# Kernel tuning notes

Measured on AMD Instinct MI355X. Metric: run time of the kernel, lower is better.

Reference implementation:

```python
import jax, jax.numpy as jnp
import numpy as np


def setup_inputs() -> dict:
    key = jax.random.key(0)
    k1, k2 = jax.random.split(key)
    x = jax.random.normal(k1, (32, 512, 512, 1), dtype=jnp.float32)
    se = jnp.ones((3, 3), dtype=jnp.float32)
    rank = jax.random.normal(k2, (9,), dtype=jnp.float32)
    return {"x": x, "se": se, "rank": rank}


def _extract_patches_3x3_same(x):
    # x: [B, H, W, 1] -> [B, H, W, 9], zero-padded SAME, row-major window order
    B, H, W, C = x.shape
    xp = jnp.pad(x, ((0, 0), (1, 1), (1, 1), (0, 0)))
    shifts = [xp[:, dy:dy + H, dx:dx + W, 0] for dy in range(3) for dx in range(3)]
    return jnp.stack(shifts, axis=-1)  # [B, H, W, 9]


def reference(x, se, rank):
    # Faithful to Morph2D.call: patches * se, sort ascending over the 9-window,
    # softmax(rank)-weighted sum -> soft rank-order filter.
    patches = _extract_patches_3x3_same(x)              # [B,H,W,9]
    weighted = patches * se.reshape(9)                  # elementwise by SE
    sorted_p = jnp.sort(weighted, axis=-1)              # ascending over window
    w = jax.nn.softmax(rank)                            # [9]
    out = jnp.sum(sorted_p * w, axis=-1)                # [B,H,W]
    return out.reshape(x.shape)                         # [B,H,W,1]
```

## Files before the change

### kernel.cpp

```cpp
#include <hip/hip_runtime.h>


#define HH 512
#define WW 512

#define RFL(x) __int_as_float(__builtin_amdgcn_readfirstlane(__float_as_int(x)))
#define MIN3(a,b,c) fminf(fminf(a,b),c)
#define MAX3(a,b,c) fmaxf(fmaxf(a,b),c)
#define MED3(a,b,c) __builtin_amdgcn_fmed3f(a,b,c)
#define TSORT(a,b,c) { float t0_=MIN3(a,b,c), t1_=MED3(a,b,c), t2_=MAX3(a,b,c); a=t0_; b=t1_; c=t2_; }

__global__ __launch_bounds__(256) void morph2d_kernel(
    const float* __restrict__ x, const float* __restrict__ se9,
    const float* __restrict__ rank, float* __restrict__ out)
{
    int nper = gridDim.x >> 3;
    int lb   = (blockIdx.x & 7) * nper + (blockIdx.x >> 3);
    int g    = lb * 256 + threadIdx.x;

    int gx = g & 127;
    int rg = (g >> 7) & 127;
    int b  = g >> 14;
    int x4 = gx << 2;
    int y0 = rg << 2;
    int lane = threadIdx.x & 63;

    const float* img = x + (size_t)b * (HH * WW);

    int   rowoff[6];
    float mm[6];
    #pragma unroll
    for (int r = 0; r < 6; ++r) {
        int ry = y0 - 1 + r;
        rowoff[r] = min(max(ry, 0), HH - 1) * WW;
        mm[r]     = (ry >= 0 && ry < HH) ? 1.f : 0.f;
    }

    float4 c[6];
    #pragma unroll
    for (int r = 0; r < 6; ++r)
        c[r] = *(const float4*)(img + rowoff[r] + x4);

    bool eL = (lane == 0)  && (x4 > 0);
    bool eR = (lane == 63) && (x4 + 4 < WW);
    float eg[6] = {0.f, 0.f, 0.f, 0.f, 0.f, 0.f};
    if (eL || eR) {
        int eoff = eL ? (x4 - 1) : (x4 + 4);
        #pragma unroll
        for (int r = 0; r < 6; ++r)
            eg[r] = img[rowoff[r] + eoff];
    }

    float w0,w1,w2,w3,w4,w5,w6,w7,w8;
    float s0,s1,s2,s3,s4,s5,s6,s7,s8;
    {
        float e[9]; float s = 0.f;
        #pragma unroll
        for (int i = 0; i < 9; ++i) { e[i] = __expf(rank[i]); s += e[i]; }
        float inv = 1.0f / s;
        w0=RFL(e[0]*inv); w1=RFL(e[1]*inv); w2=RFL(e[2]*inv);
        w3=RFL(e[3]*inv); w4=RFL(e[4]*inv); w5=RFL(e[5]*inv);
        w6=RFL(e[6]*inv); w7=RFL(e[7]*inv); w8=RFL(e[8]*inv);
        s0=RFL(se9[0]); s1=RFL(se9[1]); s2=RFL(se9[2]); s3=RFL(se9[3]);
        s4=RFL(se9[4]); s5=RFL(se9[5]); s6=RFL(se9[6]); s7=RFL(se9[7]); s8=RFL(se9[8]);
    }

    float R[6][6];
    #pragma unroll
    for (int r = 0; r < 6; ++r) {
        float lw = __shfl_up(c[r].w, 1);
        float rx = __shfl_down(c[r].x, 1);
        float lf = (lane == 0)  ? eg[r] : lw;
        float rt = (lane == 63) ? eg[r] : rx;
        float m  = mm[r];
        R[r][0] = lf * m;     R[r][1] = c[r].x * m; R[r][2] = c[r].y * m;
        R[r][3] = c[r].z * m; R[r][4] = c[r].w * m; R[r][5] = rt * m;
    }

    #pragma unroll
    for (int r = 0; r < 4; ++r) {
        float res[4];
        #pragma unroll
        for (int j = 0; j < 4; ++j) {
            float v0 = R[r  ][j]*s0, v1 = R[r  ][j+1]*s1, v2 = R[r  ][j+2]*s2;
            float v3 = R[r+1][j]*s3, v4 = R[r+1][j+1]*s4, v5 = R[r+1][j+2]*s5;
            float v6 = R[r+2][j]*s6, v7 = R[r+2][j+1]*s7, v8 = R[r+2][j+2]*s8;

            TSORT(v0, v1, v2)
            TSORT(v3, v4, v5)
            TSORT(v6, v7, v8)
            TSORT(v0, v3, v6)
            TSORT(v1, v4, v7)
            TSORT(v2, v5, v8)
            float r1 = fminf(v1, v3), p = fmaxf(v1, v3);
            float r7 = fmaxf(v5, v7), q = fminf(v5, v7);
            TSORT(v2, v4, v6)
            float r2 = fminf(p, v2), r3 = fmaxf(p, v2);
            float r5 = fminf(q, v6), r6 = fmaxf(q, v6);

            float acc = v0 * w0;
            acc = fmaf(r1, w1, acc);
            acc = fmaf(r2, w2, acc);
            acc = fmaf(r3, w3, acc);
            acc = fmaf(v4, w4, acc);
            acc = fmaf(r5, w5, acc);
            acc = fmaf(r6, w6, acc);
            acc = fmaf(r7, w7, acc);
            acc = fmaf(v8, w8, acc);
            res[j] = acc;
        }
        float4 o = { res[0], res[1], res[2], res[3] };
        *(float4*)(out + (((size_t)b * HH + (y0 + r)) * WW + x4)) = o;
    }
}

extern "C" void kernel_launch(void* const* d_in, const int* in_sizes, int n_in,
                              void* d_out, int out_size, void* d_ws, size_t ws_size,
                              hipStream_t stream) {
    const float* x    = (const float*)d_in[0];
    const float* se   = (const float*)d_in[1];
    const float* rank = (const float*)d_in[2];
    float* out = (float*)d_out;

    const int total_threads = 32 * (HH / 4) * (WW / 4);
    morph2d_kernel<<<total_threads / 256, 256, 0, stream>>>(x, se, rank, out);
}
```

Baseline: 90.17 us.

## Add uniform-SE fast path sharing column sorts across adjacent outputs

Adds a branch, taken when all nine structuring-element values are equal and positive, that pulls the scale out of the sort and folds it into the softmax weights. In that branch each column of three is sorted once and the result is shared by the overlapping windows, so each output pixel needs only the row sorts and the final merge. The per-row multiply by a validity mask is replaced by zeroing the top or bottom halo row only at the image edges. The general path is kept for non-uniform SE values, at the cost of more code size and a few uniform comparisons per thread.

```diff
diff --git a/kernel.cpp b/kernel.cpp
--- a/kernel.cpp
+++ b/kernel.cpp
@@ -27,13 +27,11 @@
 
     const float* img = x + (size_t)b * (HH * WW);
 
-    int   rowoff[6];
-    float mm[6];
+    int rowoff[6];
     #pragma unroll
     for (int r = 0; r < 6; ++r) {
         int ry = y0 - 1 + r;
         rowoff[r] = min(max(ry, 0), HH - 1) * WW;
-        mm[r]     = (ry >= 0 && ry < HH) ? 1.f : 0.f;
     }
 
     float4 c[6];
@@ -72,45 +70,102 @@
         float rx = __shfl_down(c[r].x, 1);
         float lf = (lane == 0)  ? eg[r] : lw;
         float rt = (lane == 63) ? eg[r] : rx;
-        float m  = mm[r];
-        R[r][0] = lf * m;     R[r][1] = c[r].x * m; R[r][2] = c[r].y * m;
-        R[r][3] = c[r].z * m; R[r][4] = c[r].w * m; R[r][5] = rt * m;
+        R[r][0] = lf;     R[r][1] = c[r].x; R[r][2] = c[r].y;
+        R[r][3] = c[r].z; R[r][4] = c[r].w; R[r][5] = rt;
     }
 
-    #pragma unroll
-    for (int r = 0; r < 4; ++r) {
-        float res[4];
+    if (y0 == 0) {
         #pragma unroll
-        for (int j = 0; j < 4; ++j) {
-            float v0 = R[r  ][j]*s0, v1 = R[r  ][j+1]*s1, v2 = R[r  ][j+2]*s2;
-            float v3 = R[r+1][j]*s3, v4 = R[r+1][j+1]*s4, v5 = R[r+1][j+2]*s5;
-            float v6 = R[r+2][j]*s6, v7 = R[r+2][j+1]*s7, v8 = R[r+2][j+2]*s8;
+        for (int cc = 0; cc < 6; ++cc) R[0][cc] = 0.f;
+    }
+    if (y0 == HH - 4) {
+        #pragma unroll
+        for (int cc = 0; cc < 6; ++cc) R[5][cc] = 0.f;
+    }
 
-            TSORT(v0, v1, v2)
-            TSORT(v3, v4, v5)
-            TSORT(v6, v7, v8)
-            TSORT(v0, v3, v6)
-            TSORT(v1, v4, v7)
-            TSORT(v2, v5, v8)
-            float r1 = fminf(v1, v3), p = fmaxf(v1, v3);
-            float r7 = fmaxf(v5, v7), q = fminf(v5, v7);
-            TSORT(v2, v4, v6)
-            float r2 = fminf(p, v2), r3 = fmaxf(p, v2);
-            float r5 = fminf(q, v6), r6 = fmaxf(q, v6);
+    bool uni = (s0==s1) && (s1==s2) && (s2==s3) && (s3==s4) &&
+               (s4==s5) && (s5==s6) && (s6==s7) && (s7==s8) && (s0 > 0.f);
 
-            float acc = v0 * w0;
-            acc = fmaf(r1, w1, acc);
-            acc = fmaf(r2, w2, acc);
-            acc = fmaf(r3, w3, acc);
-            acc = fmaf(v4, w4, acc);
-            acc = fmaf(r5, w5, acc);
-            acc = fmaf(r6, w6, acc);
-            acc = fmaf(r7, w7, acc);
-            acc = fmaf(v8, w8, acc);
-            res[j] = acc;
+    if (uni) {
+        float W0=RFL(w0*s0), W1=RFL(w1*s0), W2=RFL(w2*s0);
+        float W3=RFL(w3*s0), W4=RFL(w4*s0), W5=RFL(w5*s0);
+        float W6=RFL(w6*s0), W7=RFL(w7*s0), W8=RFL(w8*s0);
+
+        #pragma unroll
+        for (int r = 0; r < 4; ++r) {
+            float cs0[6], cs1[6], cs2[6];
+            #pragma unroll
+            for (int cc = 0; cc < 6; ++cc) {
+                float u0 = R[r][cc], u1 = R[r+1][cc], u2 = R[r+2][cc];
+                TSORT(u0, u1, u2)
+                cs0[cc] = u0; cs1[cc] = u1; cs2[cc] = u2;
+            }
+            float res[4];
+            #pragma unroll
+            for (int j = 0; j < 4; ++j) {
+                float v0 = cs0[j], v1 = cs0[j+1], v2 = cs0[j+2];
+                float v3 = cs1[j], v4 = cs1[j+1], v5 = cs1[j+2];
+                float v6 = cs2[j], v7 = cs2[j+1], v8 = cs2[j+2];
+
+                TSORT(v0, v1, v2)
+                TSORT(v3, v4, v5)
+                TSORT(v6, v7, v8)
+                float r1 = fminf(v1, v3), p = fmaxf(v1, v3);
+                float r7 = fmaxf(v5, v7), q = fminf(v5, v7);
+                TSORT(v2, v4, v6)
+                float r2 = fminf(p, v2), r3 = fmaxf(p, v2);
+                float r5 = fminf(q, v6), r6 = fmaxf(q, v6);
+
+                float acc = v0 * W0;
+                acc = fmaf(r1, W1, acc);
+                acc = fmaf(r2, W2, acc);
+                acc = fmaf(r3, W3, acc);
+                acc = fmaf(v4, W4, acc);
+                acc = fmaf(r5, W5, acc);
+                acc = fmaf(r6, W6, acc);
+                acc = fmaf(r7, W7, acc);
+                acc = fmaf(v8, W8, acc);
+                res[j] = acc;
+            }
+            float4 o = { res[0], res[1], res[2], res[3] };
+            *(float4*)(out + (((size_t)b * HH + (y0 + r)) * WW + x4)) = o;
         }
-        float4 o = { res[0], res[1], res[2], res[3] };
-        *(float4*)(out + (((size_t)b * HH + (y0 + r)) * WW + x4)) = o;
+    } else {
+        #pragma unroll
+        for (int r = 0; r < 4; ++r) {
+            float res[4];
+            #pragma unroll
+            for (int j = 0; j < 4; ++j) {
+                float v0 = R[r  ][j]*s0, v1 = R[r  ][j+1]*s1, v2 = R[r  ][j+2]*s2;
+                float v3 = R[r+1][j]*s3, v4 = R[r+1][j+1]*s4, v5 = R[r+1][j+2]*s5;
+                float v6 = R[r+2][j]*s6, v7 = R[r+2][j+1]*s7, v8 = R[r+2][j+2]*s8;
+
+                TSORT(v0, v1, v2)
+                TSORT(v3, v4, v5)
+                TSORT(v6, v7, v8)
+                TSORT(v0, v3, v6)
+                TSORT(v1, v4, v7)
+                TSORT(v2, v5, v8)
+                float r1 = fminf(v1, v3), p = fmaxf(v1, v3);
+                float r7 = fmaxf(v5, v7), q = fminf(v5, v7);
+                TSORT(v2, v4, v6)
+                float r2 = fminf(p, v2), r3 = fmaxf(p, v2);
+                float r5 = fminf(q, v6), r6 = fmaxf(q, v6);
+
+                float acc = v0 * w0;
+                acc = fmaf(r1, w1, acc);
+                acc = fmaf(r2, w2, acc);
+                acc = fmaf(r3, w3, acc);
+                acc = fmaf(v4, w4, acc);
+                acc = fmaf(r5, w5, acc);
+                acc = fmaf(r6, w6, acc);
+                acc = fmaf(r7, w7, acc);
+                acc = fmaf(v8, w8, acc);
+                res[j] = acc;
+            }
+            float4 o = { res[0], res[1], res[2], res[3] };
+            *(float4*)(out + (((size_t)b * HH + (y0 + r)) * WW + x4)) = o;
+        }
     }
 }
 
```

New measurement: 88.83 us (median of 2 runs). No clear change (-1.5%).
